# Optimization experiments

Hardware: AMD Instinct MI355X
Metric: run time of the kernel (lower is better)

## Reference

```python
import jax, jax.numpy as jnp
import numpy as np

CONST = 0.0  # init kwarg `const`


def setup_inputs() -> dict:
    key = jax.random.key(0)
    kx, = jax.random.split(key, 1)
    B, C, H, W = 16, 1, 2048, 2048
    x = jax.random.normal(kx, (B, C, H, W), dtype=jnp.float32)
    a = jnp.ones((3,), dtype=jnp.float32)   # stencil params: center, horiz, vert
    w = jnp.ones((4,), dtype=jnp.float32)   # polynomial coeffs w0..w3 (poly_order=3)
    return {"x": x, "a": a, "w": w}


def reference(x, a, w):
    # Replicate-pad H and W by 1 (== F.pad(x, (1,1,1,1), 'replicate'))
    xp = jnp.pad(x, ((0, 0), (0, 0), (1, 1), (1, 1)), mode="edge")
    # 5-point stencil conv: kernel center=a0, left/right=a1, up/down=a2, corners=0.
    # Expressed as shifted adds instead of a dense conv (same math, one memory pass).
    center = x
    horiz = xp[:, :, 1:-1, :-2] + xp[:, :, 1:-1, 2:]   # left + right neighbors
    vert = xp[:, :, :-2, 1:-1] + xp[:, :, 2:, 1:-1]    # up + down neighbors
    stencil = a[0] * center + a[1] * horiz + a[2] * vert
    # Polynomial p = w0 + w1*d + w2*d^2 + w3*d^3 with d = x - const (Horner form)
    d = x - CONST
    p = w[3]
    p = p * d + w[2]
    p = p * d + w[1]
    p = p * d + w[0]
    return stencil + p
```

## Files before the change

### kernel.cpp

```cpp
#include <hip/hip_runtime.h>


#define H_DIM 2048
#define W_DIM 2048
#define W4    (W_DIM / 4)
#define RPT   8
#define BLK   256

typedef float fvec4 __attribute__((ext_vector_type(4)));

__global__ __launch_bounds__(BLK) void FCNN_63651415326860_kernel(
    const float* __restrict__ x,
    const float* __restrict__ a,
    const float* __restrict__ w,
    float* __restrict__ out)
{
    const int chunk = gridDim.x >> 3;
    const int swz   = (blockIdx.x & 7) * chunk + (blockIdx.x >> 3);

    const int half = swz & 1;
    const int band = swz >> 1;

    const int col4 = half * BLK + (int)threadIdx.x;
    const int lane = threadIdx.x & 63;

    const int rowg0 = band * RPT;
    const int row0  = rowg0 & (H_DIM - 1);

    const float4* __restrict__ x4 = (const float4*)x;

    const float a0 = a[0], a1 = a[1], a2 = a[2];
    const float w0 = w[0], w1 = w[1], w2 = w[2], w3 = w[3];

    int v = rowg0 * W4 + col4;

    float4 cur = x4[v];
    float4 up  = (row0 == 0) ? cur : x4[v - W4];

    #pragma unroll
    for (int r = 0; r < RPT; ++r) {
        const int row = row0 + r;
        const float4 dn = (row == H_DIM - 1) ? cur : x4[v + W4];

        float lw = __shfl(cur.w, (lane > 0)  ? lane - 1 : 0);
        float rw = __shfl(cur.x, (lane < 63) ? lane + 1 : 63);
        if (lane == 0)
            lw = (col4 == 0)      ? cur.x : x[(size_t)v * 4 - 1];
        if (lane == 63)
            rw = (col4 == W4 - 1) ? cur.w : x[(size_t)v * 4 + 4];

        fvec4 res;
        res.x = a0 * cur.x + a1 * (lw    + cur.y) + a2 * (up.x + dn.x)
              + fmaf(fmaf(fmaf(w3, cur.x, w2), cur.x, w1), cur.x, w0);
        res.y = a0 * cur.y + a1 * (cur.x + cur.z) + a2 * (up.y + dn.y)
              + fmaf(fmaf(fmaf(w3, cur.y, w2), cur.y, w1), cur.y, w0);
        res.z = a0 * cur.z + a1 * (cur.y + cur.w) + a2 * (up.z + dn.z)
              + fmaf(fmaf(fmaf(w3, cur.z, w2), cur.z, w1), cur.z, w0);
        res.w = a0 * cur.w + a1 * (cur.z + rw   ) + a2 * (up.w + dn.w)
              + fmaf(fmaf(fmaf(w3, cur.w, w2), cur.w, w1), cur.w, w0);

        __builtin_nontemporal_store(res, (fvec4*)(out + (size_t)v * 4));

        up = cur;
        cur = dn;
        v += W4;
    }
}

extern "C" void kernel_launch(void* const* d_in, const int* in_sizes, int n_in,
                              void* d_out, int out_size, void* d_ws, size_t ws_size,
                              hipStream_t stream) {
    const float* x = (const float*)d_in[0];
    const float* a = (const float*)d_in[1];
    const float* w = (const float*)d_in[2];
    float* out = (float*)d_out;

    const int total4 = out_size / 4;
    const int grid = total4 / (BLK * RPT);

    FCNN_63651415326860_kernel<<<grid, BLK, 0, stream>>>(x, a, w, out);
}
```

Before: 456.8 us.

## Prefetch rows two ahead, load halo scalars directly, double rows per thread

Each thread now processes 16 rows instead of 8. It software-pipelines loads two rows ahead and handles two output rows per iteration. Left and right halo values now come from direct scalar global loads instead of wave shuffles, and the nontemporal store becomes a regular store. Launch bounds request 8 blocks per CU. The aim is more memory-level parallelism and less shuffle overhead, at the cost of more registers, redundant scalar loads that mostly hit cache, and possibly more cache pollution on stores.

```diff
diff --git a/kernel.cpp b/kernel.cpp
--- a/kernel.cpp
+++ b/kernel.cpp
@@ -4,12 +4,12 @@
 #define H_DIM 2048
 #define W_DIM 2048
 #define W4    (W_DIM / 4)
-#define RPT   8
+#define CH    16
 #define BLK   256
 
 typedef float fvec4 __attribute__((ext_vector_type(4)));
 
-__global__ __launch_bounds__(BLK) void FCNN_63651415326860_kernel(
+__global__ __launch_bounds__(BLK, 8) void FCNN_63651415326860_kernel(
     const float* __restrict__ x,
     const float* __restrict__ a,
     const float* __restrict__ w,
@@ -21,50 +21,70 @@
     const int half = swz & 1;
     const int band = swz >> 1;
 
-    const int col4 = half * BLK + (int)threadIdx.x;
-    const int lane = threadIdx.x & 63;
-
-    const int rowg0 = band * RPT;
+    const int col4  = half * BLK + (int)threadIdx.x;
+    const int rowg0 = band * CH;
     const int row0  = rowg0 & (H_DIM - 1);
 
     const float4* __restrict__ x4 = (const float4*)x;
+    const int v0 = rowg0 * W4 + col4;
+
+    const bool top = (row0 == 0);
+    const bool bot = (row0 + CH == H_DIM);
+
+    const int s0   = v0 * 4;
+    const int offL = (col4 != 0)      ? s0 - 1 : s0;
+    const int offR = (col4 != W4 - 1) ? s0 + 4 : s0 + 3;
 
     const float a0 = a[0], a1 = a[1], a2 = a[2];
     const float w0 = w[0], w1 = w[1], w2 = w[2], w3 = w[3];
 
-    int v = rowg0 * W4 + col4;
+    #define RIDX(k) (bot ? (((k) > CH - 1) ? CH - 1 : (k)) : (k))
 
-    float4 cur = x4[v];
-    float4 up  = (row0 == 0) ? cur : x4[v - W4];
+    #define ROW(up_, cur_, dn_, lw_, rw_, vi_)                                  \
+    {                                                                           \
+        fvec4 res_;                                                             \
+        res_.x = a0 * (cur_).x + a1 * ((lw_)    + (cur_).y)                     \
+               + a2 * ((up_).x + (dn_).x)                                       \
+               + fmaf(fmaf(fmaf(w3, (cur_).x, w2), (cur_).x, w1), (cur_).x, w0);\
+        res_.y = a0 * (cur_).y + a1 * ((cur_).x + (cur_).z)                     \
+               + a2 * ((up_).y + (dn_).y)                                       \
+               + fmaf(fmaf(fmaf(w3, (cur_).y, w2), (cur_).y, w1), (cur_).y, w0);\
+        res_.z = a0 * (cur_).z + a1 * ((cur_).y + (cur_).w)                     \
+               + a2 * ((up_).z + (dn_).z)                                       \
+               + fmaf(fmaf(fmaf(w3, (cur_).z, w2), (cur_).z, w1), (cur_).z, w0);\
+        res_.w = a0 * (cur_).w + a1 * ((cur_).z + (rw_))                        \
+               + a2 * ((up_).w + (dn_).w)                                       \
+               + fmaf(fmaf(fmaf(w3, (cur_).w, w2), (cur_).w, w1), (cur_).w, w0);\
+        *(fvec4*)(out + (size_t)(vi_) * 4) = res_;                              \
+    }
+
+    float4 A = x4[top ? v0 : v0 - W4];
+    float4 B = x4[v0];
+    float4 C = x4[v0 + W4];
+    float4 D = x4[v0 + RIDX(2) * W4];
+    float lw0 = x[offL],          rw0 = x[offR];
+    float lw1 = x[offL + W_DIM],  rw1 = x[offR + W_DIM];
 
     #pragma unroll
-    for (int r = 0; r < RPT; ++r) {
-        const int row = row0 + r;
-        const float4 dn = (row == H_DIM - 1) ? cur : x4[v + W4];
+    for (int r = 0; r < CH; r += 2) {
+        float4 E = D, F = D;
+        float lw2 = lw0, rw2 = rw0, lw3 = lw0, rw3 = rw0;
+        if (r + 3 <= CH)     E   = x4[v0 + RIDX(r + 3) * W4];
+        if (r + 4 <= CH)     F   = x4[v0 + RIDX(r + 4) * W4];
+        if (r + 2 <= CH - 1) { lw2 = x[offL + RIDX(r + 2) * W_DIM];
+                               rw2 = x[offR + RIDX(r + 2) * W_DIM]; }
+        if (r + 3 <= CH - 1) { lw3 = x[offL + RIDX(r + 3) * W_DIM];
+                               rw3 = x[offR + RIDX(r + 3) * W_DIM]; }
 
-        float lw = __shfl(cur.w, (lane > 0)  ? lane - 1 : 0);
-        float rw = __shfl(cur.x, (lane < 63) ? lane + 1 : 63);
-        if (lane == 0)
-            lw = (col4 == 0)      ? cur.x : x[(size_t)v * 4 - 1];
-        if (lane == 63)
-            rw = (col4 == W4 - 1) ? cur.w : x[(size_t)v * 4 + 4];
+        ROW(A, B, C, lw0, rw0, v0 + r * W4);
+        ROW(B, C, D, lw1, rw1, v0 + (r + 1) * W4);
 
-        fvec4 res;
-        res.x = a0 * cur.x + a1 * (lw    + cur.y) + a2 * (up.x + dn.x)
-              + fmaf(fmaf(fmaf(w3, cur.x, w2), cur.x, w1), cur.x, w0);
-        res.y = a0 * cur.y + a1 * (cur.x + cur.z) + a2 * (up.y + dn.y)
-              + fmaf(fmaf(fmaf(w3, cur.y, w2), cur.y, w1), cur.y, w0);
-        res.z = a0 * cur.z + a1 * (cur.y + cur.w) + a2 * (up.z + dn.z)
-              + fmaf(fmaf(fmaf(w3, cur.z, w2), cur.z, w1), cur.z, w0);
-        res.w = a0 * cur.w + a1 * (cur.z + rw   ) + a2 * (up.w + dn.w)
-              + fmaf(fmaf(fmaf(w3, cur.w, w2), cur.w, w1), cur.w, w0);
+        A = C; B = D; C = E; D = F;
+        lw0 = lw2; rw0 = rw2; lw1 = lw3; rw1 = rw3;
+    }
 
-        __builtin_nontemporal_store(res, (fvec4*)(out + (size_t)v * 4));
-
-        up = cur;
-        cur = dn;
-        v += W4;
-    }
+    #undef ROW
+    #undef RIDX
 }
 
 extern "C" void kernel_launch(void* const* d_in, const int* in_sizes, int n_in,
@@ -76,7 +96,7 @@
     float* out = (float*)d_out;
 
     const int total4 = out_size / 4;
-    const int grid = total4 / (BLK * RPT);
+    const int grid = total4 / (BLK * CH);
 
     FCNN_63651415326860_kernel<<<grid, BLK, 0, stream>>>(x, a, w, out);
 }
```

Result: faster. 441.7 us (-3.3%).
